# Performance work log

Hardware: AMD Instinct MI355X
Metric: run time of the kernel (lower is better)

The kernel has to match this reference:

```python
import jax, jax.numpy as jnp
import numpy as np

K_SIZE = 3      # kernel height/width
STRIDE = 1
SPARSITY = 0.7  # fraction of zero weights in the kernel


def setup_inputs() -> dict:
    key = jax.random.key(0)
    k1, k2, k3 = jax.random.split(key, 3)
    N, C, H, W = 32, 128, 56, 56
    F = 256
    Kdim = C * K_SIZE * K_SIZE  # 1152
    inputs = jax.random.normal(k1, (N, C, H, W), dtype=jnp.float32)
    limit = np.sqrt(6.0 / (F + Kdim)).astype(np.float32)
    vals = jax.random.uniform(k2, (F, Kdim), dtype=jnp.float32, minval=-limit, maxval=limit)
    mask = (jax.random.uniform(k3, (F, Kdim)) >= SPARSITY).astype(jnp.float32)
    kernel = vals * mask
    return {"inputs": inputs, "kernel": kernel}


def reference(inputs, kernel):
    k, s = K_SIZE, STRIDE
    # Original: transpose NCHW -> (N, W, H, C), extract_patches over (W, H)
    x = jnp.transpose(inputs, (0, 3, 2, 1))  # (N, W, H, C)
    N, Wd, Hd, C = x.shape
    Wo = (Wd - k) // s + 1
    Ho = (Hd - k) // s + 1
    # im2col: patch flatten order = [w_offset, h_offset, channel], matching tf.image.extract_patches
    patches = jnp.stack(
        [x[:, i : i + (Wo - 1) * s + 1 : s, j : j + (Ho - 1) * s + 1 : s, :]
         for i in range(k) for j in range(k)],
        axis=3,
    )  # (N, Wo, Ho, k*k, C)
    flat = patches.reshape(N, Wo, Ho, k * k * C)
    # CSR spmm == dense matmul with the (structurally sparse) dense kernel
    out = jnp.einsum('nwhk,fk->nfwh', flat, kernel)  # (N, F, Wo, Ho)
    return out
```

## Files before the change

### kernel.cpp

```cpp
#include <hip/hip_runtime.h>

typedef _Float16 half8 __attribute__((ext_vector_type(8)));
typedef float f32x16 __attribute__((ext_vector_type(16)));

#define N_IMG 32
#define C_IN  128
#define H_IN  56
#define W_IN  56
#define F_OUT 256
#define HO    54
#define WO    54
#define KKDIM 1152
#define NKB   18

#define T2_BYTES (N_IMG * W_IN * H_IN * C_IN * 2)
#define BP_OFF   T2_BYTES
#define BP_BYTES (NKB * F_OUT * 64 * 2)
#define WS_NEED  (BP_OFF + BP_BYTES)

#define SLAB_I_STRIDE 14336
#define A_REGION  88576
#define B_CHUNK   32768
#define SMEM_BYTES (A_REGION + 2 * B_CHUNK)

#define ASM_BAR() asm volatile("s_barrier" ::: "memory")

static __device__ inline unsigned pack2(float a, float b) {
    union { _Float16 h[2]; unsigned u; } x;
    x.h[0] = (_Float16)a; x.h[1] = (_Float16)b; return x.u;
}

__global__ __launch_bounds__(256) void k_transpose(const float* __restrict__ in,
                                                   _Float16* __restrict__ t2) {
    __shared__ char Lt[4 * 56 * 256];
    const int n   = blockIdx.y;
    const int hh0 = blockIdx.x * 4;
    const int t   = threadIdx.x;
    const int lane = t & 63, wid = t >> 6;
    const float4* in4 = (const float4*)in;

    if (lane < 56) {
        const int ww4 = lane % 14, hhi = lane / 14;
        const int X    = lane & 15;
        const int rowb = (hhi * 56 + ww4 * 4) * 256;
        const int gbase = ((n * 128) * 56 + hh0 + hhi) * 14 + ww4;
#pragma unroll 4
        for (int p = 0; p < 16; ++p) {
            const int c0 = wid * 32 + p * 2;
            float4 a = in4[gbase + c0 * 56 * 14];
            float4 b = in4[gbase + (c0 + 1) * 56 * 14];
            const int cb = c0 * 2;
            const int swz = (cb & 15) | ((((cb >> 4)) ^ X) << 4);
            const float* af = (const float*)&a;
            const float* bf = (const float*)&b;
#pragma unroll
            for (int i = 0; i < 4; ++i)
                *(unsigned*)(Lt + rowb + i * 256 + swz) = pack2(af[i], bf[i]);
        }
    }
    __syncthreads();

    {
        const int j = t & 15;
        int ww = t >> 4, hhi = 0;
        for (int it = 0; it < 14; ++it) {
            const int X  = (hhi * 14 + (ww >> 2)) & 15;
            const int hh = hh0 + hhi;
            const int s  = j ^ (hh & 15) ^ X;
            int4 v = *(const int4*)(Lt + (hhi * 56 + ww) * 256 + s * 16);
            char* dst = (char*)t2 + ((size_t)((n * 56 + ww) * 56 + hh)) * 256 + j * 16;
            *(int4*)dst = v;
            ww += 16; if (ww >= 56) { ww -= 56; ++hhi; }
        }
    }
}

__global__ __launch_bounds__(256) void k_weights(const float* __restrict__ kern,
                                                 _Float16* __restrict__ bp) {
    const int tid = blockIdx.x * 256 + threadIdx.x;
    if (tid >= F_OUT * KKDIM / 4) return;
    const float4 v = ((const float4*)kern)[tid];
    const int kq = tid % 288, f = tid / 288;
    const int kb   = kq >> 4;
    const int kin2 = (kq & 15) * 8;
    uint2 w; w.x = pack2(v.x, v.y); w.y = pack2(v.z, v.w);
    char* dst = (char*)bp + kb * B_CHUNK + f * 128
              + ((kin2 & 15) | (((kin2 >> 4) ^ (f & 7)) << 4));
    *(uint2*)dst = w;
}

typedef const __attribute__((address_space(1))) unsigned int guint;
typedef __attribute__((address_space(3))) unsigned int luint;

#define LDA_(S, A0, A1) do { \
    const int cb_ = ch2 + (S)*32 + kin2; \
    A0 = *(const half8*)(As + abase + (cb_ ^ Xa)); \
    A1 = *(const half8*)(As + abase + 8192 + (cb_ ^ Xa)); } while(0)

#define LDB_(S, B0, B1, B2, B3) do { \
    const int ob_ = (((S)*32 + kin2) ^ Xb); \
    B0 = *(const half8*)(curB + fb128 + ob_); \
    B1 = *(const half8*)(curB + fb128 + 4096 + ob_); \
    B2 = *(const half8*)(curB + fb128 + 8192 + ob_); \
    B3 = *(const half8*)(curB + fb128 + 12288 + ob_); } while(0)

#define MM_(A0, A1, B0, B1, B2, B3) do { \
    __builtin_amdgcn_s_setprio(1); \
    acc[0][0] = __builtin_amdgcn_mfma_f32_32x32x16_f16(B0, A0, acc[0][0], 0, 0, 0); \
    acc[1][0] = __builtin_amdgcn_mfma_f32_32x32x16_f16(B0, A1, acc[1][0], 0, 0, 0); \
    acc[0][1] = __builtin_amdgcn_mfma_f32_32x32x16_f16(B1, A0, acc[0][1], 0, 0, 0); \
    acc[1][1] = __builtin_amdgcn_mfma_f32_32x32x16_f16(B1, A1, acc[1][1], 0, 0, 0); \
    acc[0][2] = __builtin_amdgcn_mfma_f32_32x32x16_f16(B2, A0, acc[0][2], 0, 0, 0); \
    acc[1][2] = __builtin_amdgcn_mfma_f32_32x32x16_f16(B2, A1, acc[1][2], 0, 0, 0); \
    acc[0][3] = __builtin_amdgcn_mfma_f32_32x32x16_f16(B3, A0, acc[0][3], 0, 0, 0); \
    acc[1][3] = __builtin_amdgcn_mfma_f32_32x32x16_f16(B3, A1, acc[1][3], 0, 0, 0); \
    __builtin_amdgcn_s_setprio(0); } while(0)

__global__ __launch_bounds__(512, 2) void k_gemm(const _Float16* __restrict__ t2,
                                                 const _Float16* __restrict__ bp,
                                                 float* __restrict__ out) {
    extern __shared__ char smem[];
    char* As  = smem;
    char* Bs0 = smem + A_REGION;
    char* Bs1 = smem + A_REGION + B_CHUNK;

    const int tid  = threadIdx.x;
    const int lane = tid & 63;
    const int wid  = tid >> 6;
    const int wm   = wid >> 1;
    const int wf   = wid & 1;
    const int ln31 = lane & 31;
    const int kin2 = (lane >> 5) * 16;
    const int n  = blockIdx.y;
    const int w0 = blockIdx.x * 4;

    int navail = 56 - w0; if (navail > 6) navail = 6;
    const int bytesA = navail * SLAB_I_STRIDE;
    const char* t2n = (const char*)t2 + (size_t)(n * 56 + w0) * 56 * 256;
    for (int o = tid * 16; o < bytesA; o += 8192)
        __builtin_amdgcn_global_load_lds((guint*)(t2n + o), (luint*)(As + o), 16, 0, 0);

    const char* bpc = (const char*)bp;
#pragma unroll
    for (int q = 0; q < 4; ++q)
        __builtin_amdgcn_global_load_lds((guint*)(bpc + tid * 16 + q * 8192),
                                         (luint*)(Bs0 + tid * 16 + q * 8192), 16, 0, 0);

    f32x16 acc[2][4];
#pragma unroll
    for (int m2 = 0; m2 < 2; ++m2)
#pragma unroll
        for (int ft = 0; ft < 4; ++ft)
#pragma unroll
            for (int e = 0; e < 16; ++e)
                acc[m2][ft][e] = 0.0f;

    asm volatile("s_waitcnt vmcnt(0)" ::: "memory");
    ASM_BAR();

    const int Xb = (ln31 & 7) << 4;
    const int fb128 = (wf * 128 + ln31) * 128;

    for (int kb = 0; kb < NKB; ++kb) {
        const char* curB = (kb & 1) ? Bs1 : Bs0;
        if (kb < NKB - 1) {
            char* nxtB = (kb & 1) ? Bs0 : Bs1;
            const char* src = bpc + (kb + 1) * B_CHUNK;
#pragma unroll
            for (int q = 0; q < 4; ++q)
                __builtin_amdgcn_global_load_lds((guint*)(src + tid * 16 + q * 8192),
                                                 (luint*)(nxtB + tid * 16 + q * 8192), 16, 0, 0);
            asm volatile("s_waitcnt vmcnt(4)" ::: "memory");
        } else {
            asm volatile("s_waitcnt vmcnt(0)" ::: "memory");
        }
        ASM_BAR();

        const int ij  = kb >> 1;
        const int iq  = ij / 3;
        const int jq  = ij - iq * 3;
        const int ch2 = (kb & 1) * 128;
        const int hh0 = ln31 + jq;
        const int Xa  = (hh0 & 15) << 4;
        const int abase = (wm + iq) * SLAB_I_STRIDE + hh0 * 256;

        half8 xa0, xa1, xb0, xb1, xb2, xb3;
        half8 ya0, ya1, yb0, yb1, yb2, yb3;
        LDA_(0, xa0, xa1); LDB_(0, xb0, xb1, xb2, xb3);
        LDA_(1, ya0, ya1); LDB_(1, yb0, yb1, yb2, yb3);
        MM_(xa0, xa1, xb0, xb1, xb2, xb3);
        LDA_(2, xa0, xa1); LDB_(2, xb0, xb1, xb2, xb3);
        MM_(ya0, ya1, yb0, yb1, yb2, yb3);
        LDA_(3, ya0, ya1); LDB_(3, yb0, yb1, yb2, yb3);
        MM_(xa0, xa1, xb0, xb1, xb2, xb3);
        MM_(ya0, ya1, yb0, yb1, yb2, yb3);

        ASM_BAR();
    }

    const int w = w0 + wm;
    if (w < WO) {
        float* opb = out + ((size_t)(n * 256 + wf * 128) * 54 + w) * 54;
        const int f4 = (lane >> 5) * 4;
#pragma unroll
        for (int m2 = 0; m2 < 2; ++m2) {
            const int h = m2 * 32 + ln31;
            if (h < HO) {
#pragma unroll
                for (int ft = 0; ft < 4; ++ft) {
#pragma unroll
                    for (int e = 0; e < 16; ++e) {
                        const int fl = ft * 32 + (e & 3) + 8 * (e >> 2) + f4;
                        opb[(size_t)fl * 2916 + h] = acc[m2][ft][e];
                    }
                }
            }
        }
    }
}

__global__ __launch_bounds__(256) void k_naive(const float* __restrict__ in,
                                               const float* __restrict__ kern,
                                               float* __restrict__ out) {
    const int idx = blockIdx.x * 256 + threadIdx.x;
    const int total = N_IMG * F_OUT * WO * HO;
    if (idx >= total) return;
    const int h = idx % 54;
    const int w = (idx / 54) % 54;
    const int f = (idx / (54 * 54)) % 256;
    const int n = idx / (54 * 54 * 256);
    float s = 0.f;
    for (int ij = 0; ij < 9; ++ij) {
        const int i = ij / 3, j = ij % 3;
        const float* ip = in + ((size_t)(n * 128) * 56 + (h + j)) * 56 + (w + i);
        const float* kp = kern + (size_t)f * KKDIM + ij * 128;
        for (int c = 0; c < 128; ++c) s += ip[(size_t)c * 3136] * kp[c];
    }
    out[idx] = s;
}

extern "C" void kernel_launch(void* const* d_in, const int* in_sizes, int n_in,
                              void* d_out, int out_size, void* d_ws, size_t ws_size,
                              hipStream_t stream) {
    const float* in   = (const float*)d_in[0];
    const float* kern = (const float*)d_in[1];
    float* out = (float*)d_out;

    if (ws_size < (size_t)WS_NEED) {
        const int total = N_IMG * F_OUT * WO * HO;
        k_naive<<<(total + 255) / 256, 256, 0, stream>>>(in, kern, out);
        return;
    }

    _Float16* t2 = (_Float16*)d_ws;
    _Float16* bp = (_Float16*)((char*)d_ws + BP_OFF);

    k_transpose<<<dim3(14, 32), 256, 0, stream>>>(in, t2);
    k_weights<<<288, 256, 0, stream>>>(kern, bp);

    (void)hipFuncSetAttribute((const void*)k_gemm,
                              hipFuncAttributeMaxDynamicSharedMemorySize, SMEM_BYTES);
    k_gemm<<<dim3(14, 32), 512, SMEM_BYTES, stream>>>(t2, bp, out);
}
```

Measured before the change: 223.9 us.

## Load GEMM weight fragments directly from global memory instead of LDS double-buffering

The GEMM kernel no longer stages weight tiles through a double-buffered LDS region. Each wave now reads its B fragments straight from global memory into registers for each k-block. This removes the per-iteration barriers and waitcnts and shrinks shared memory to just the input slab. The MFMA operand order is swapped so each lane holds four consecutive output rows, which allows vectorized 16-byte stores along h. The trade-off is that global or L2 load latency is now exposed inside the k-loop with no explicit prefetch, and the weight layout loses its XOR swizzle.

```diff
diff --git a/kernel.cpp b/kernel.cpp
--- a/kernel.cpp
+++ b/kernel.cpp
@@ -2,6 +2,7 @@
 
 typedef _Float16 half8 __attribute__((ext_vector_type(8)));
 typedef float f32x16 __attribute__((ext_vector_type(16)));
+typedef float f32x4 __attribute__((ext_vector_type(4)));
 
 #define N_IMG 32
 #define C_IN  128
@@ -21,7 +22,7 @@
 #define SLAB_I_STRIDE 14336
 #define A_REGION  88576
 #define B_CHUNK   32768
-#define SMEM_BYTES (A_REGION + 2 * B_CHUNK)
+#define SMEM_BYTES A_REGION
 
 #define ASM_BAR() asm volatile("s_barrier" ::: "memory")
 
@@ -84,45 +85,18 @@
     const int kb   = kq >> 4;
     const int kin2 = (kq & 15) * 8;
     uint2 w; w.x = pack2(v.x, v.y); w.y = pack2(v.z, v.w);
-    char* dst = (char*)bp + kb * B_CHUNK + f * 128
-              + ((kin2 & 15) | (((kin2 >> 4) ^ (f & 7)) << 4));
+    char* dst = (char*)bp + kb * B_CHUNK + f * 128 + kin2;
     *(uint2*)dst = w;
 }
 
 typedef const __attribute__((address_space(1))) unsigned int guint;
 typedef __attribute__((address_space(3))) unsigned int luint;
-
-#define LDA_(S, A0, A1) do { \
-    const int cb_ = ch2 + (S)*32 + kin2; \
-    A0 = *(const half8*)(As + abase + (cb_ ^ Xa)); \
-    A1 = *(const half8*)(As + abase + 8192 + (cb_ ^ Xa)); } while(0)
-
-#define LDB_(S, B0, B1, B2, B3) do { \
-    const int ob_ = (((S)*32 + kin2) ^ Xb); \
-    B0 = *(const half8*)(curB + fb128 + ob_); \
-    B1 = *(const half8*)(curB + fb128 + 4096 + ob_); \
-    B2 = *(const half8*)(curB + fb128 + 8192 + ob_); \
-    B3 = *(const half8*)(curB + fb128 + 12288 + ob_); } while(0)
-
-#define MM_(A0, A1, B0, B1, B2, B3) do { \
-    __builtin_amdgcn_s_setprio(1); \
-    acc[0][0] = __builtin_amdgcn_mfma_f32_32x32x16_f16(B0, A0, acc[0][0], 0, 0, 0); \
-    acc[1][0] = __builtin_amdgcn_mfma_f32_32x32x16_f16(B0, A1, acc[1][0], 0, 0, 0); \
-    acc[0][1] = __builtin_amdgcn_mfma_f32_32x32x16_f16(B1, A0, acc[0][1], 0, 0, 0); \
-    acc[1][1] = __builtin_amdgcn_mfma_f32_32x32x16_f16(B1, A1, acc[1][1], 0, 0, 0); \
-    acc[0][2] = __builtin_amdgcn_mfma_f32_32x32x16_f16(B2, A0, acc[0][2], 0, 0, 0); \
-    acc[1][2] = __builtin_amdgcn_mfma_f32_32x32x16_f16(B2, A1, acc[1][2], 0, 0, 0); \
-    acc[0][3] = __builtin_amdgcn_mfma_f32_32x32x16_f16(B3, A0, acc[0][3], 0, 0, 0); \
-    acc[1][3] = __builtin_amdgcn_mfma_f32_32x32x16_f16(B3, A1, acc[1][3], 0, 0, 0); \
-    __builtin_amdgcn_s_setprio(0); } while(0)
 
 __global__ __launch_bounds__(512, 2) void k_gemm(const _Float16* __restrict__ t2,
                                                  const _Float16* __restrict__ bp,
                                                  float* __restrict__ out) {
     extern __shared__ char smem[];
-    char* As  = smem;
-    char* Bs0 = smem + A_REGION;
-    char* Bs1 = smem + A_REGION + B_CHUNK;
+    char* As = smem;
 
     const int tid  = threadIdx.x;
     const int lane = tid & 63;
@@ -140,12 +114,6 @@
     for (int o = tid * 16; o < bytesA; o += 8192)
         __builtin_amdgcn_global_load_lds((guint*)(t2n + o), (luint*)(As + o), 16, 0, 0);
 
-    const char* bpc = (const char*)bp;
-#pragma unroll
-    for (int q = 0; q < 4; ++q)
-        __builtin_amdgcn_global_load_lds((guint*)(bpc + tid * 16 + q * 8192),
-                                         (luint*)(Bs0 + tid * 16 + q * 8192), 16, 0, 0);
-
     f32x16 acc[2][4];
 #pragma unroll
     for (int m2 = 0; m2 < 2; ++m2)
@@ -158,24 +126,10 @@
     asm volatile("s_waitcnt vmcnt(0)" ::: "memory");
     ASM_BAR();
 
-    const int Xb = (ln31 & 7) << 4;
-    const int fb128 = (wf * 128 + ln31) * 128;
+    const char* bpc = (const char*)bp;
+    const char* bl  = bpc + (wf * 128 + ln31) * 128 + kin2;
 
     for (int kb = 0; kb < NKB; ++kb) {
-        const char* curB = (kb & 1) ? Bs1 : Bs0;
-        if (kb < NKB - 1) {
-            char* nxtB = (kb & 1) ? Bs0 : Bs1;
-            const char* src = bpc + (kb + 1) * B_CHUNK;
-#pragma unroll
-            for (int q = 0; q < 4; ++q)
-                __builtin_amdgcn_global_load_lds((guint*)(src + tid * 16 + q * 8192),
-                                                 (luint*)(nxtB + tid * 16 + q * 8192), 16, 0, 0);
-            asm volatile("s_waitcnt vmcnt(4)" ::: "memory");
-        } else {
-            asm volatile("s_waitcnt vmcnt(0)" ::: "memory");
-        }
-        ASM_BAR();
-
         const int ij  = kb >> 1;
         const int iq  = ij / 3;
         const int jq  = ij - iq * 3;
@@ -183,35 +137,49 @@
         const int hh0 = ln31 + jq;
         const int Xa  = (hh0 & 15) << 4;
         const int abase = (wm + iq) * SLAB_I_STRIDE + hh0 * 256;
-
-        half8 xa0, xa1, xb0, xb1, xb2, xb3;
-        half8 ya0, ya1, yb0, yb1, yb2, yb3;
-        LDA_(0, xa0, xa1); LDB_(0, xb0, xb1, xb2, xb3);
-        LDA_(1, ya0, ya1); LDB_(1, yb0, yb1, yb2, yb3);
-        MM_(xa0, xa1, xb0, xb1, xb2, xb3);
-        LDA_(2, xa0, xa1); LDB_(2, xb0, xb1, xb2, xb3);
-        MM_(ya0, ya1, yb0, yb1, yb2, yb3);
-        LDA_(3, ya0, ya1); LDB_(3, yb0, yb1, yb2, yb3);
-        MM_(xa0, xa1, xb0, xb1, xb2, xb3);
-        MM_(ya0, ya1, yb0, yb1, yb2, yb3);
-
-        ASM_BAR();
+        const char* bk = bl + kb * B_CHUNK;
+
+        half8 bF[4][4];
+#pragma unroll
+        for (int s = 0; s < 4; ++s)
+#pragma unroll
+            for (int ft = 0; ft < 4; ++ft)
+                bF[s][ft] = *(const half8*)(bk + ft * 4096 + s * 32);
+
+#pragma unroll
+        for (int s = 0; s < 4; ++s) {
+            const int cb = ch2 + s * 32 + kin2;
+            half8 aF0 = *(const half8*)(As + abase + (cb ^ Xa));
+            half8 aF1 = *(const half8*)(As + abase + 8192 + (cb ^ Xa));
+            __builtin_amdgcn_s_setprio(1);
+#pragma unroll
+            for (int ft = 0; ft < 4; ++ft) {
+                acc[0][ft] = __builtin_amdgcn_mfma_f32_32x32x16_f16(aF0, bF[s][ft], acc[0][ft], 0, 0, 0);
+                acc[1][ft] = __builtin_amdgcn_mfma_f32_32x32x16_f16(aF1, bF[s][ft], acc[1][ft], 0, 0, 0);
+            }
+            __builtin_amdgcn_s_setprio(0);
+        }
     }
 
     const int w = w0 + wm;
     if (w < WO) {
-        float* opb = out + ((size_t)(n * 256 + wf * 128) * 54 + w) * 54;
-        const int f4 = (lane >> 5) * 4;
+        const int hi4 = (lane >> 5) * 4;
 #pragma unroll
         for (int m2 = 0; m2 < 2; ++m2) {
-            const int h = m2 * 32 + ln31;
-            if (h < HO) {
-#pragma unroll
-                for (int ft = 0; ft < 4; ++ft) {
-#pragma unroll
-                    for (int e = 0; e < 16; ++e) {
-                        const int fl = ft * 32 + (e & 3) + 8 * (e >> 2) + f4;
-                        opb[(size_t)fl * 2916 + h] = acc[m2][ft][e];
+#pragma unroll
+            for (int ft = 0; ft < 4; ++ft) {
+                const int f = wf * 128 + ft * 32 + ln31;
+                float* op = out + ((size_t)(n * 256 + f) * 54 + w) * 54;
+#pragma unroll
+                for (int q = 0; q < 4; ++q) {
+                    const int hb = m2 * 32 + q * 8 + hi4;
+                    if (hb + 3 < HO) {
+                        f32x4 v = { acc[m2][ft][4 * q + 0], acc[m2][ft][4 * q + 1],
+                                    acc[m2][ft][4 * q + 2], acc[m2][ft][4 * q + 3] };
+                        *(f32x4*)(op + hb) = v;
+                    } else if (hb < HO) {
+                        op[hb]     = acc[m2][ft][4 * q + 0];
+                        op[hb + 1] = acc[m2][ft][4 * q + 1];
                     }
                 }
             }
```

New measurement: 292.2 us. 1.31x slower.
